# Kernel optimization log

Measured on AMD Instinct MI355X. Metric: run time of the kernel, lower is better.

## Reference

```python
import jax, jax.numpy as jnp
import numpy as np

N_ATOMS = 393216   # 4096 molecules * ~96 atoms
N_FEAT = 128
NB_FILTER = 128
NB_AFFINE = 11     # max_deg(10) + 1 - min_deg(0)
BATCH = 4096


def setup_inputs() -> dict:
    key = jax.random.key(0)
    k1, k2, k3, k4 = jax.random.split(key, 4)
    atoms = jax.random.normal(k1, (N_ATOMS, N_FEAT), jnp.float32)
    # stacked per-degree affine weights (glorot-ish scale)
    W = jax.random.normal(k2, (NB_AFFINE, N_FEAT, NB_FILTER), jnp.float32) / jnp.sqrt(jnp.float32(N_FEAT))
    b = jax.random.normal(k3, (NB_AFFINE, NB_FILTER), jnp.float32) * 0.01
    # contiguous degree layout: deg_slice[k] = (start, count), atoms sorted by degree
    counts = np.full(NB_AFFINE, N_ATOMS // NB_AFFINE, dtype=np.int32)
    counts[-1] += N_ATOMS - counts.sum()
    starts = np.concatenate([[0], np.cumsum(counts)[:-1]]).astype(np.int32)
    deg_slice = jnp.asarray(np.stack([starts, counts], axis=1))  # (11, 2) int32
    membership = jax.random.randint(k4, (N_ATOMS,), 0, BATCH, dtype=jnp.int32)
    return {"atoms": atoms, "W": W, "b": b, "deg_slice": deg_slice,
            "membership": membership, "batch_size": BATCH}


def reference(atoms, W, b, deg_slice, membership, batch_size):
    # atoms: (N, F); W: (K, F, O); b: (K, O); deg_slice: (K, 2)
    n = atoms.shape[0]
    nb_affine = W.shape[0]
    # Per-atom degree index from contiguous deg_slice layout:
    # deg_idx[i] = number of degree blocks that end at or before atom i.
    ends = jnp.cumsum(deg_slice[:, 1])                     # (K,)
    idx = jnp.arange(n, dtype=ends.dtype)
    deg_idx = jnp.sum(idx[:, None] >= ends[None, :], axis=1)  # (N,)
    # Per-degree affine: each atom uses the (W, b) of its degree block.
    out = jnp.zeros((n, W.shape[2]), dtype=atoms.dtype)
    for k in range(nb_affine):  # fixed small structural loop (11 distinct weight sets)
        yk = atoms @ W[k] + b[k]
        out = out + jnp.where((deg_idx == k)[:, None], yk, jnp.zeros((), atoms.dtype))
    # graph_gather: dynamic_partition + per-partition reduce_sum + concat == segment_sum
    pooled = jax.ops.segment_sum(out, membership, num_segments=batch_size)  # (B, O)
    # activation is 'linear' (identity); dropout is None
    return pooled
```

## Files before the change

kernel.cpp:

```cpp
#include <hip/hip_runtime.h>
#include <hip/hip_bf16.h>


#define CAP 64

typedef short bf16x8 __attribute__((ext_vector_type(8)));
typedef float f32x4  __attribute__((ext_vector_type(4)));

__device__ __forceinline__ unsigned short f2bf(float f) {
    unsigned int u = __builtin_bit_cast(unsigned int, f);
    u += 0x7fffu + ((u >> 16) & 1u);
    return (unsigned short)(u >> 16);
}

__device__ __forceinline__ int deg_of(int i, const int* __restrict__ ds, int K) {
    int k = 0, end = 0;
    for (int kk = 0; kk < K; ++kk) { end += ds[2 * kk + 1]; k += (i >= end) ? 1 : 0; }
    return k;
}

__global__ __launch_bounds__(256) void k_fill_wconv(
    const int* __restrict__ mem, const int* __restrict__ ds,
    const float* __restrict__ W,
    unsigned* __restrict__ cnt, unsigned* __restrict__ slots,
    unsigned short* __restrict__ Wb, int N, int K, int nb)
{
    int bx = blockIdx.x;
    if (bx >= nb) {
        __shared__ unsigned short t[128 * 130];
        int k = bx - nb;
        const float* Wk = W + (size_t)k * 16384;
        unsigned short* Wbk = Wb + (size_t)k * 16384;
        for (int e = threadIdx.x; e < 16384; e += 256) {
            int f = e >> 7, c = e & 127;
            t[f * 130 + c] = f2bf(Wk[e]);
        }
        __syncthreads();
        for (int e = threadIdx.x; e < 16384; e += 256) {
            int c = e >> 7, f = e & 127;
            Wbk[e] = t[f * 130 + c];
        }
        return;
    }
    int i = bx * 256 + threadIdx.x;
    if (i >= N) return;
    int key = mem[i] * K + deg_of(i, ds, K);
    unsigned p = atomicAdd(&cnt[key], 1u);
    if (p < CAP) slots[(size_t)key * CAP + p] = (unsigned)i;
}

__device__ __forceinline__ float4 f4add(float4 a, float4 b) {
    return make_float4(a.x + b.x, a.y + b.y, a.z + b.z, a.w + b.w);
}

__global__ __launch_bounds__(256) void k_phaseA(
    const float* __restrict__ atoms,
    const unsigned* __restrict__ cnt,
    const unsigned* __restrict__ slots,
    unsigned short* __restrict__ S, int KB)
{
    int bin = blockIdx.x * 4 + (threadIdx.x >> 6);
    if (bin >= KB) return;
    int lane = threadIdx.x & 63;
    int rpar = lane >> 5;
    int f4   = lane & 31;
    int n = (int)cnt[bin];
    if (n > CAP) n = CAP;
    const unsigned* sl = slots + (size_t)bin * CAP;

    float4 A0 = make_float4(0.f, 0.f, 0.f, 0.f);
    float4 A1 = A0, A2 = A0, A3 = A0;
    int j = rpar;
    for (; j + 6 < n; j += 8) {
        unsigned r0 = sl[j], r1 = sl[j + 2], r2 = sl[j + 4], r3 = sl[j + 6];
        float4 v0 = *reinterpret_cast<const float4*>(atoms + (size_t)r0 * 128 + f4 * 4);
        float4 v1 = *reinterpret_cast<const float4*>(atoms + (size_t)r1 * 128 + f4 * 4);
        float4 v2 = *reinterpret_cast<const float4*>(atoms + (size_t)r2 * 128 + f4 * 4);
        float4 v3 = *reinterpret_cast<const float4*>(atoms + (size_t)r3 * 128 + f4 * 4);
        A0 = f4add(A0, v0); A1 = f4add(A1, v1);
        A2 = f4add(A2, v2); A3 = f4add(A3, v3);
    }
    for (; j < n; j += 2) {
        float4 v = *reinterpret_cast<const float4*>(atoms + (size_t)sl[j] * 128 + f4 * 4);
        A0 = f4add(A0, v);
    }
    float4 Sm = f4add(f4add(A0, A1), f4add(A2, A3));
    Sm.x += __shfl_xor(Sm.x, 32, 64);
    Sm.y += __shfl_xor(Sm.y, 32, 64);
    Sm.z += __shfl_xor(Sm.z, 32, 64);
    Sm.w += __shfl_xor(Sm.w, 32, 64);
    if (rpar == 0) {
        unsigned lo = (unsigned)f2bf(Sm.x) | ((unsigned)f2bf(Sm.y) << 16);
        unsigned hi = (unsigned)f2bf(Sm.z) | ((unsigned)f2bf(Sm.w) << 16);
        *reinterpret_cast<uint2*>(S + (size_t)bin * 128 + f4 * 4) = make_uint2(lo, hi);
    }
}

__global__ __launch_bounds__(64) void k_phaseB(
    const unsigned short* __restrict__ S,
    const unsigned short* __restrict__ Wb,
    const unsigned* __restrict__ cnt,
    const float* __restrict__ bias,
    float* __restrict__ out,
    int K)
{
    int bx   = blockIdx.x;
    int s0   = (bx >> 2) * 16;
    int c0   = (bx & 3) * 32;
    int lane = threadIdx.x;
    int quad = lane >> 4, cb = lane & 15;

    const int KD = K * 128;
    f32x4 acc0 = (f32x4){0.f, 0.f, 0.f, 0.f};
    f32x4 acc1 = (f32x4){0.f, 0.f, 0.f, 0.f};

    const unsigned short* Arow = S  + (size_t)(s0 + cb) * KD + quad * 8;
    const unsigned short* B0   = Wb + (size_t)(c0 + cb)      * 128 + quad * 8;
    const unsigned short* B1   = Wb + (size_t)(c0 + 16 + cb) * 128 + quad * 8;

    #pragma unroll 1
    for (int kk = 0; kk < K; ++kk) {
        #pragma unroll
        for (int k0 = 0; k0 < 128; k0 += 32) {
            bf16x8 a  = *reinterpret_cast<const bf16x8*>(Arow + kk * 128 + k0);
            bf16x8 b0 = *reinterpret_cast<const bf16x8*>(B0 + (size_t)kk * 16384 + k0);
            bf16x8 b1 = *reinterpret_cast<const bf16x8*>(B1 + (size_t)kk * 16384 + k0);
            acc0 = __builtin_amdgcn_mfma_f32_16x16x32_bf16(a, b0, acc0, 0, 0, 0);
            acc1 = __builtin_amdgcn_mfma_f32_16x16x32_bf16(a, b1, acc1, 0, 0, 0);
        }
    }
    #pragma unroll
    for (int reg = 0; reg < 4; ++reg) {
        int s = s0 + quad * 4 + reg;
        float b0s = 0.f, b1s = 0.f;
        for (int k = 0; k < K; ++k) {
            float c = (float)cnt[(size_t)s * K + k];
            b0s += c * bias[k * 128 + c0 + cb];
            b1s += c * bias[k * 128 + c0 + 16 + cb];
        }
        out[(size_t)s * 128 + c0 + cb]      = acc0[reg] + b0s;
        out[(size_t)s * 128 + c0 + 16 + cb] = acc1[reg] + b1s;
    }
}

#define TM 64
#define LDA 136
#define LDW 136
__global__ __launch_bounds__(256, 2) void degree_affine_pool(
    const float* __restrict__ atoms, const float* __restrict__ W,
    const float* __restrict__ bias, const int* __restrict__ deg_slice,
    const int* __restrict__ membership, float* __restrict__ out, int K)
{
    __shared__ unsigned short Alds[TM * LDA];
    __shared__ unsigned short Wlds[128 * LDW];
    const int bid = blockIdx.x, tid = threadIdx.x;
    int k = -1, tile = 0, acc_t = 0;
    for (int kk = 0; kk < K; ++kk) {
        int c = deg_slice[2 * kk + 1];
        int nt = (c + TM - 1) >> 6;
        if (k < 0 && bid < acc_t + nt) { k = kk; tile = bid - acc_t; }
        acc_t += nt;
    }
    if (k < 0) return;
    const int start = deg_slice[2 * k], cnt = deg_slice[2 * k + 1];
    const int row0 = start + tile * TM;
    const int rows_valid = min(TM, cnt - tile * TM);
    for (int e = tid; e < TM * 32; e += 256) {
        int r = e >> 5, f4 = e & 31;
        float4 v = make_float4(0.f, 0.f, 0.f, 0.f);
        if (r < rows_valid)
            v = *reinterpret_cast<const float4*>(atoms + (size_t)(row0 + r) * 128 + f4 * 4);
        unsigned lo = (unsigned)f2bf(v.x) | ((unsigned)f2bf(v.y) << 16);
        unsigned hi = (unsigned)f2bf(v.z) | ((unsigned)f2bf(v.w) << 16);
        *reinterpret_cast<uint2*>(&Alds[r * LDA + f4 * 4]) = make_uint2(lo, hi);
    }
    const float* Wk = W + (size_t)k * 16384;
    for (int e = tid; e < 8192; e += 256) {
        int c = e & 127, f2 = e >> 7;
        unsigned p = (unsigned)f2bf(Wk[(2 * f2) * 128 + c]) |
                     ((unsigned)f2bf(Wk[(2 * f2 + 1) * 128 + c]) << 16);
        *reinterpret_cast<unsigned*>(&Wlds[c * LDW + 2 * f2]) = p;
    }
    __syncthreads();
    const int wave = tid >> 6, lane = tid & 63, quad = lane >> 4, cb = lane & 15;
    f32x4 acc[8];
    #pragma unroll
    for (int ct = 0; ct < 8; ++ct) acc[ct] = (f32x4){0.f, 0.f, 0.f, 0.f};
    #pragma unroll
    for (int k0 = 0; k0 < 128; k0 += 32) {
        bf16x8 af = *reinterpret_cast<const bf16x8*>(&Alds[(wave * 16 + cb) * LDA + k0 + quad * 8]);
        #pragma unroll
        for (int ct = 0; ct < 8; ++ct) {
            bf16x8 bf = *reinterpret_cast<const bf16x8*>(&Wlds[(ct * 16 + cb) * LDW + k0 + quad * 8]);
            acc[ct] = __builtin_amdgcn_mfma_f32_16x16x32_bf16(af, bf, acc[ct], 0, 0, 0);
        }
    }
    int segs[4]; bool valid[4];
    #pragma unroll
    for (int reg = 0; reg < 4; ++reg) {
        int rl = wave * 16 + quad * 4 + reg;
        valid[reg] = (rl < rows_valid);
        segs[reg] = valid[reg] ? membership[row0 + rl] : 0;
    }
    const float* bk = bias + k * 128;
    #pragma unroll
    for (int ct = 0; ct < 8; ++ct) {
        int col = ct * 16 + cb;
        float bv = bk[col];
        #pragma unroll
        for (int reg = 0; reg < 4; ++reg)
            if (valid[reg])
                __hip_atomic_fetch_add(out + (size_t)segs[reg] * 128 + col,
                                       acc[ct][reg] + bv, __ATOMIC_RELAXED,
                                       __HIP_MEMORY_SCOPE_AGENT);
    }
}

static inline size_t aln(size_t x) { return (x + 255) & ~(size_t)255; }

extern "C" void kernel_launch(void* const* d_in, const int* in_sizes, int n_in,
                              void* d_out, int out_size, void* d_ws, size_t ws_size,
                              hipStream_t stream) {
    const float* atoms = (const float*)d_in[0];
    const float* W     = (const float*)d_in[1];
    const float* bias  = (const float*)d_in[2];
    const int*   deg   = (const int*)d_in[3];
    const int*   mem   = (const int*)d_in[4];
    float*       out   = (float*)d_out;

    const int K  = in_sizes[3] / 2;
    const int N  = in_sizes[0] / 128;
    const int B  = out_size / 128;
    const int KB = B * K;

    size_t oWb   = 0;                       size_t sWb   = (size_t)K * 16384 * 2;
    size_t oCnt  = aln(oWb + sWb);          size_t sCnt  = (size_t)KB * 4;
    size_t oSlot = aln(oCnt + sCnt);        size_t sSlot = (size_t)KB * CAP * 4;
    size_t oS    = aln(oSlot + sSlot);      size_t sS    = (size_t)KB * 128 * 2;
    size_t total = oS + sS;

    if (ws_size < total || (B & 15) != 0) {
        (void)hipMemsetAsync(d_out, 0, (size_t)out_size * sizeof(float), stream);
        const int blocks = (N + TM - 1) / TM + K;
        degree_affine_pool<<<blocks, 256, 0, stream>>>(atoms, W, bias, deg, mem, out, K);
        return;
    }

    char* ws = (char*)d_ws;
    unsigned short* Wb    = (unsigned short*)(ws + oWb);
    unsigned*       cnt   = (unsigned*)(ws + oCnt);
    unsigned*       slots = (unsigned*)(ws + oSlot);
    unsigned short* S     = (unsigned short*)(ws + oS);

    (void)hipMemsetAsync(cnt, 0, sCnt, stream);

    const int nb = (N + 255) / 256;
    k_fill_wconv<<<nb + K, 256, 0, stream>>>(mem, deg, W, cnt, slots, Wb, N, K, nb);
    k_phaseA    <<<(KB + 3) / 4, 256, 0, stream>>>(atoms, cnt, slots, S, KB);
    k_phaseB    <<<(B / 16) * 4, 64, 0, stream>>>(S, Wb, cnt, bias, out, K);
}
```

Before: 347.1 us.

## Merge bin, gather, and GEMM phases into one cooperative persistent kernel

Replaces the memset and three separate launches with a single cooperative-launch kernel that uses grid-wide syncs between phases: zeroing counts, binning atoms, converting weights plus gathering bin sums, then an MFMA GEMM with bias folded in from the counts. The aim is to remove launch and inter-kernel gaps. The GEMM phase also writes directly instead of using atomics. The grid is capped at 1024 blocks, so each phase has less parallelism, and the grid syncs add cost. It falls back to the old path if cooperative launch is unavailable.

```diff
diff --git a/kernel.cpp b/kernel.cpp
--- a/kernel.cpp
+++ b/kernel.cpp
@@ -1,5 +1,8 @@
 #include <hip/hip_runtime.h>
 #include <hip/hip_bf16.h>
+#include <hip/hip_cooperative_groups.h>
+
+namespace cg = cooperative_groups;
 
 
 #define CAP 64
@@ -17,6 +20,119 @@
     int k = 0, end = 0;
     for (int kk = 0; kk < K; ++kk) { end += ds[2 * kk + 1]; k += (i >= end) ? 1 : 0; }
     return k;
+}
+
+__device__ __forceinline__ float4 f4add(float4 a, float4 b) {
+    return make_float4(a.x + b.x, a.y + b.y, a.z + b.z, a.w + b.w);
+}
+
+__global__ __launch_bounds__(256, 4) void k_merged(
+    const float* __restrict__ atoms, const float* __restrict__ W,
+    const float* __restrict__ bias, const int* __restrict__ ds,
+    const int* __restrict__ mem,
+    unsigned* __restrict__ cnt, unsigned* __restrict__ slots,
+    unsigned short* __restrict__ Wb, unsigned short* __restrict__ S,
+    float* __restrict__ out, int N, int K, int B, int KB)
+{
+    cg::grid_group gg = cg::this_grid();
+    const int tid  = threadIdx.x;
+    const int gtid = blockIdx.x * 256 + tid;
+    const int gsz  = gridDim.x * 256;
+    const int lane = tid & 63;
+
+    for (int i = gtid; i < KB; i += gsz) cnt[i] = 0u;
+    __threadfence();
+    gg.sync();
+
+    for (int i = gtid; i < N; i += gsz) {
+        int key = mem[i] * K + deg_of(i, ds, K);
+        unsigned p = atomicAdd(&cnt[key], 1u);
+        if (p < CAP) slots[(size_t)key * CAP + p] = (unsigned)i;
+    }
+    __threadfence();
+    gg.sync();
+
+    if (blockIdx.x < (unsigned)K) {
+        __shared__ unsigned short t[128 * 130];
+        const float* Wk = W + (size_t)blockIdx.x * 16384;
+        unsigned short* Wbk = Wb + (size_t)blockIdx.x * 16384;
+        for (int e = tid; e < 16384; e += 256)
+            t[(e >> 7) * 130 + (e & 127)] = f2bf(Wk[e]);
+        __syncthreads();
+        for (int e = tid; e < 16384; e += 256)
+            Wbk[e] = t[(e & 127) * 130 + (e >> 7)];
+    }
+
+    {
+        const int gw   = gtid >> 6;
+        const int nw   = gsz >> 6;
+        const int rpar = lane >> 5;
+        const int f4   = lane & 31;
+        const int bpw  = (KB + nw - 1) / nw;
+        for (int t = 0; t < bpw; ++t) {
+            const int bin = gw * bpw + t;
+            if (bin >= KB) break;
+            int n = (int)cnt[bin];
+            if (n > CAP) n = CAP;
+            const unsigned* sl = slots + (size_t)bin * CAP;
+            float4 A0 = make_float4(0.f, 0.f, 0.f, 0.f);
+            float4 A1 = A0, A2 = A0, A3 = A0;
+            int j = rpar;
+            for (; j + 6 < n; j += 8) {
+                unsigned r0 = sl[j], r1 = sl[j + 2], r2 = sl[j + 4], r3 = sl[j + 6];
+                A0 = f4add(A0, *reinterpret_cast<const float4*>(atoms + (size_t)r0 * 128 + f4 * 4));
+                A1 = f4add(A1, *reinterpret_cast<const float4*>(atoms + (size_t)r1 * 128 + f4 * 4));
+                A2 = f4add(A2, *reinterpret_cast<const float4*>(atoms + (size_t)r2 * 128 + f4 * 4));
+                A3 = f4add(A3, *reinterpret_cast<const float4*>(atoms + (size_t)r3 * 128 + f4 * 4));
+            }
+            for (; j < n; j += 2)
+                A0 = f4add(A0, *reinterpret_cast<const float4*>(atoms + (size_t)sl[j] * 128 + f4 * 4));
+            float4 Sm = f4add(f4add(A0, A1), f4add(A2, A3));
+            Sm.x += __shfl_xor(Sm.x, 32, 64);
+            Sm.y += __shfl_xor(Sm.y, 32, 64);
+            Sm.z += __shfl_xor(Sm.z, 32, 64);
+            Sm.w += __shfl_xor(Sm.w, 32, 64);
+            if (rpar == 0) {
+                unsigned lo = (unsigned)f2bf(Sm.x) | ((unsigned)f2bf(Sm.y) << 16);
+                unsigned hi = (unsigned)f2bf(Sm.z) | ((unsigned)f2bf(Sm.w) << 16);
+                *reinterpret_cast<uint2*>(S + (size_t)bin * 128 + f4 * 4) = make_uint2(lo, hi);
+            }
+        }
+    }
+    __threadfence();
+    gg.sync();
+
+    {
+        const int gw = gtid >> 6;
+        const int nw = gsz >> 6;
+        const int quad = lane >> 4, cb = lane & 15;
+        const int KD = K * 128;
+        const int ntiles = (B >> 4) * 8;
+        for (int tile = gw; tile < ntiles; tile += nw) {
+            const int s0 = (tile >> 3) << 4;
+            const int c0 = (tile & 7) << 4;
+            f32x4 acc = (f32x4){0.f, 0.f, 0.f, 0.f};
+            const unsigned short* Arow = S  + (size_t)(s0 + cb) * KD + quad * 8;
+            const unsigned short* Bp   = Wb + (size_t)(c0 + cb) * 128 + quad * 8;
+            #pragma unroll 1
+            for (int kk = 0; kk < K; ++kk) {
+                #pragma unroll
+                for (int k0 = 0; k0 < 128; k0 += 32) {
+                    bf16x8 a = *reinterpret_cast<const bf16x8*>(Arow + kk * 128 + k0);
+                    bf16x8 b = *reinterpret_cast<const bf16x8*>(Bp + (size_t)kk * 16384 + k0);
+                    acc = __builtin_amdgcn_mfma_f32_16x16x32_bf16(a, b, acc, 0, 0, 0);
+                }
+            }
+            #pragma unroll
+            for (int reg = 0; reg < 4; ++reg) {
+                const int s = s0 + quad * 4 + reg;
+                float bs = 0.f;
+                for (int k = 0; k < K; ++k)
+                    bs += (float)cnt[(size_t)s * K + k] * bias[k * 128 + c0 + cb];
+                out[(size_t)s * 128 + c0 + cb] = acc[reg] + bs;
+            }
+        }
+    }
 }
 
 __global__ __launch_bounds__(256) void k_fill_wconv(
@@ -47,10 +163,6 @@
     int key = mem[i] * K + deg_of(i, ds, K);
     unsigned p = atomicAdd(&cnt[key], 1u);
     if (p < CAP) slots[(size_t)key * CAP + p] = (unsigned)i;
-}
-
-__device__ __forceinline__ float4 f4add(float4 a, float4 b) {
-    return make_float4(a.x + b.x, a.y + b.y, a.z + b.z, a.w + b.w);
 }
 
 __global__ __launch_bounds__(256) void k_phaseA(
@@ -101,8 +213,7 @@
     const unsigned short* __restrict__ Wb,
     const unsigned* __restrict__ cnt,
     const float* __restrict__ bias,
-    float* __restrict__ out,
-    int K)
+    float* __restrict__ out, int K)
 {
     int bx   = blockIdx.x;
     int s0   = (bx >> 2) * 16;
@@ -226,7 +337,7 @@
     const float* bias  = (const float*)d_in[2];
     const int*   deg   = (const int*)d_in[3];
     const int*   mem   = (const int*)d_in[4];
-    float*       out   = (float*)d_out;
+    float*       outp  = (float*)d_out;
 
     const int K  = in_sizes[3] / 2;
     const int N  = in_sizes[0] / 128;
@@ -242,7 +353,7 @@
     if (ws_size < total || (B & 15) != 0) {
         (void)hipMemsetAsync(d_out, 0, (size_t)out_size * sizeof(float), stream);
         const int blocks = (N + TM - 1) / TM + K;
-        degree_affine_pool<<<blocks, 256, 0, stream>>>(atoms, W, bias, deg, mem, out, K);
+        degree_affine_pool<<<blocks, 256, 0, stream>>>(atoms, W, bias, deg, mem, outp, K);
         return;
     }
 
@@ -252,10 +363,36 @@
     unsigned*       slots = (unsigned*)(ws + oSlot);
     unsigned short* S     = (unsigned short*)(ws + oS);
 
+    static int s_grid = -1;
+    if (s_grid < 0) {
+        int dev = 0;  (void)hipGetDevice(&dev);
+        int coop = 0; (void)hipDeviceGetAttribute(&coop, hipDeviceAttributeCooperativeLaunch, dev);
+        int cus = 0;  (void)hipDeviceGetAttribute(&cus, hipDeviceAttributeMultiprocessorCount, dev);
+        int maxb = 0;
+        if (coop) {
+            if (hipOccupancyMaxActiveBlocksPerMultiprocessor(&maxb, k_merged, 256, 0) != hipSuccess)
+                maxb = 0;
+        }
+        int g = (coop && maxb > 0 && cus > 0) ? maxb * cus : 0;
+        if (g > 1024) g = 1024;
+        if (g < 64) g = 0;
+        s_grid = g;
+    }
+
+    if (s_grid > 0) {
+        int Np = N, Kp = K, Bp = B, KBp = KB;
+        void* args[] = { (void*)&atoms, (void*)&W, (void*)&bias, (void*)&deg, (void*)&mem,
+                         (void*)&cnt, (void*)&slots, (void*)&Wb, (void*)&S, (void*)&outp,
+                         (void*)&Np, (void*)&Kp, (void*)&Bp, (void*)&KBp };
+        if (hipLaunchCooperativeKernel(k_merged, dim3(s_grid), dim3(256),
+                                       args, 0u, stream) == hipSuccess)
+            return;
+        s_grid = 0;
+    }
+
     (void)hipMemsetAsync(cnt, 0, sCnt, stream);
-
     const int nb = (N + 255) / 256;
     k_fill_wconv<<<nb + K, 256, 0, stream>>>(mem, deg, W, cnt, slots, Wb, N, K, nb);
     k_phaseA    <<<(KB + 3) / 4, 256, 0, stream>>>(atoms, cnt, slots, S, KB);
-    k_phaseB    <<<(B / 16) * 4, 64, 0, stream>>>(S, Wb, cnt, bias, out, K);
-}
+    k_phaseB    <<<(B / 16) * 4, 64, 0, stream>>>(S, Wb, cnt, bias, outp, K);
+}
```

Result: slower. 820.1 us (+136.3%).

## Split phase-B reduction over degree halves with atomics, zero output in fill kernel

Applied to the files above, without the earlier changes.

Phase B now splits the 11-degree K loop across two blocks per output tile, doubling the grid, and accumulates into the output with relaxed float atomics. The output is zeroed by extra blocks in the fill kernel. Phase A's remainder loop is folded into a predicated main loop, and the W transpose uses half the shared memory in two passes. This trades more parallelism and occupancy for atomic traffic and an extra zeroing pass.

```diff
diff --git a/kernel.cpp b/kernel.cpp
--- a/kernel.cpp
+++ b/kernel.cpp
@@ -19,26 +19,43 @@
     return k;
 }
 
+__device__ __forceinline__ float4 f4add(float4 a, float4 b) {
+    return make_float4(a.x + b.x, a.y + b.y, a.z + b.z, a.w + b.w);
+}
+
 __global__ __launch_bounds__(256) void k_fill_wconv(
     const int* __restrict__ mem, const int* __restrict__ ds,
     const float* __restrict__ W,
     unsigned* __restrict__ cnt, unsigned* __restrict__ slots,
-    unsigned short* __restrict__ Wb, int N, int K, int nb)
+    unsigned short* __restrict__ Wb, float* __restrict__ out,
+    int N, int K, int nb, int B)
 {
     int bx = blockIdx.x;
+    if (bx >= nb + K) {
+        int zb = bx - nb - K;
+        f32x4* o4 = reinterpret_cast<f32x4*>(out);
+        int tot = (B * 128) >> 2;
+        for (int e = zb * 256 + threadIdx.x; e < tot; e += 8 * 256)
+            o4[e] = (f32x4){0.f, 0.f, 0.f, 0.f};
+        return;
+    }
     if (bx >= nb) {
-        __shared__ unsigned short t[128 * 130];
+        __shared__ unsigned short t[64 * 130];
         int k = bx - nb;
         const float* Wk = W + (size_t)k * 16384;
         unsigned short* Wbk = Wb + (size_t)k * 16384;
-        for (int e = threadIdx.x; e < 16384; e += 256) {
-            int f = e >> 7, c = e & 127;
-            t[f * 130 + c] = f2bf(Wk[e]);
-        }
-        __syncthreads();
-        for (int e = threadIdx.x; e < 16384; e += 256) {
-            int c = e >> 7, f = e & 127;
-            Wbk[e] = t[f * 130 + c];
+        #pragma unroll 1
+        for (int h = 0; h < 2; ++h) {
+            for (int e = threadIdx.x; e < 8192; e += 256) {
+                int fl = e >> 7, c = e & 127;
+                t[fl * 130 + c] = f2bf(Wk[(size_t)(h * 64 + fl) * 128 + c]);
+            }
+            __syncthreads();
+            for (int e = threadIdx.x; e < 8192; e += 256) {
+                int c = e >> 6, fl = e & 63;
+                Wbk[(size_t)c * 128 + h * 64 + fl] = t[fl * 130 + c];
+            }
+            __syncthreads();
         }
         return;
     }
@@ -47,10 +64,6 @@
     int key = mem[i] * K + deg_of(i, ds, K);
     unsigned p = atomicAdd(&cnt[key], 1u);
     if (p < CAP) slots[(size_t)key * CAP + p] = (unsigned)i;
-}
-
-__device__ __forceinline__ float4 f4add(float4 a, float4 b) {
-    return make_float4(a.x + b.x, a.y + b.y, a.z + b.z, a.w + b.w);
 }
 
 __global__ __launch_bounds__(256) void k_phaseA(
@@ -68,21 +81,23 @@
     if (n > CAP) n = CAP;
     const unsigned* sl = slots + (size_t)bin * CAP;
 
-    float4 A0 = make_float4(0.f, 0.f, 0.f, 0.f);
-    float4 A1 = A0, A2 = A0, A3 = A0;
-    int j = rpar;
-    for (; j + 6 < n; j += 8) {
-        unsigned r0 = sl[j], r1 = sl[j + 2], r2 = sl[j + 4], r3 = sl[j + 6];
+    const float4 z4 = make_float4(0.f, 0.f, 0.f, 0.f);
+    float4 A0 = z4, A1 = z4, A2 = z4, A3 = z4;
+    for (int j = rpar; j < n; j += 8) {
+        int j1 = j + 2, j2 = j + 4, j3 = j + 6;
+        unsigned r0 = sl[j];
+        unsigned r1 = sl[j1 < n ? j1 : j];
+        unsigned r2 = sl[j2 < n ? j2 : j];
+        unsigned r3 = sl[j3 < n ? j3 : j];
         float4 v0 = *reinterpret_cast<const float4*>(atoms + (size_t)r0 * 128 + f4 * 4);
         float4 v1 = *reinterpret_cast<const float4*>(atoms + (size_t)r1 * 128 + f4 * 4);
         float4 v2 = *reinterpret_cast<const float4*>(atoms + (size_t)r2 * 128 + f4 * 4);
         float4 v3 = *reinterpret_cast<const float4*>(atoms + (size_t)r3 * 128 + f4 * 4);
+        v1 = (j1 < n) ? v1 : z4;
+        v2 = (j2 < n) ? v2 : z4;
+        v3 = (j3 < n) ? v3 : z4;
         A0 = f4add(A0, v0); A1 = f4add(A1, v1);
         A2 = f4add(A2, v2); A3 = f4add(A3, v3);
-    }
-    for (; j < n; j += 2) {
-        float4 v = *reinterpret_cast<const float4*>(atoms + (size_t)sl[j] * 128 + f4 * 4);
-        A0 = f4add(A0, v);
     }
     float4 Sm = f4add(f4add(A0, A1), f4add(A2, A3));
     Sm.x += __shfl_xor(Sm.x, 32, 64);
@@ -96,7 +111,7 @@
     }
 }
 
-__global__ __launch_bounds__(64) void k_phaseB(
+__global__ __launch_bounds__(64) void k_phaseB2(
     const unsigned short* __restrict__ S,
     const unsigned short* __restrict__ Wb,
     const unsigned* __restrict__ cnt,
@@ -105,10 +120,15 @@
     int K)
 {
     int bx   = blockIdx.x;
-    int s0   = (bx >> 2) * 16;
-    int c0   = (bx & 3) * 32;
+    int s0   = (bx >> 3) * 16;
+    int c0   = ((bx >> 1) & 3) * 32;
+    int kh   = bx & 1;
     int lane = threadIdx.x;
     int quad = lane >> 4, cb = lane & 15;
+
+    const int kmid = (K + 1) / 2;
+    const int kbeg = kh ? kmid : 0;
+    const int kend = kh ? K : kmid;
 
     const int KD = K * 128;
     f32x4 acc0 = (f32x4){0.f, 0.f, 0.f, 0.f};
@@ -118,8 +138,8 @@
     const unsigned short* B0   = Wb + (size_t)(c0 + cb)      * 128 + quad * 8;
     const unsigned short* B1   = Wb + (size_t)(c0 + 16 + cb) * 128 + quad * 8;
 
-    #pragma unroll 1
-    for (int kk = 0; kk < K; ++kk) {
+    #pragma unroll 2
+    for (int kk = kbeg; kk < kend; ++kk) {
         #pragma unroll
         for (int k0 = 0; k0 < 128; k0 += 32) {
             bf16x8 a  = *reinterpret_cast<const bf16x8*>(Arow + kk * 128 + k0);
@@ -133,13 +153,17 @@
     for (int reg = 0; reg < 4; ++reg) {
         int s = s0 + quad * 4 + reg;
         float b0s = 0.f, b1s = 0.f;
-        for (int k = 0; k < K; ++k) {
-            float c = (float)cnt[(size_t)s * K + k];
-            b0s += c * bias[k * 128 + c0 + cb];
-            b1s += c * bias[k * 128 + c0 + 16 + cb];
-        }
-        out[(size_t)s * 128 + c0 + cb]      = acc0[reg] + b0s;
-        out[(size_t)s * 128 + c0 + 16 + cb] = acc1[reg] + b1s;
+        if (kh == 0) {
+            for (int k = 0; k < K; ++k) {
+                float c = (float)cnt[(size_t)s * K + k];
+                b0s += c * bias[k * 128 + c0 + cb];
+                b1s += c * bias[k * 128 + c0 + 16 + cb];
+            }
+        }
+        __hip_atomic_fetch_add(out + (size_t)s * 128 + c0 + cb, acc0[reg] + b0s,
+                               __ATOMIC_RELAXED, __HIP_MEMORY_SCOPE_AGENT);
+        __hip_atomic_fetch_add(out + (size_t)s * 128 + c0 + 16 + cb, acc1[reg] + b1s,
+                               __ATOMIC_RELAXED, __HIP_MEMORY_SCOPE_AGENT);
     }
 }
 
@@ -255,7 +279,7 @@
     (void)hipMemsetAsync(cnt, 0, sCnt, stream);
 
     const int nb = (N + 255) / 256;
-    k_fill_wconv<<<nb + K, 256, 0, stream>>>(mem, deg, W, cnt, slots, Wb, N, K, nb);
+    k_fill_wconv<<<nb + K + 8, 256, 0, stream>>>(mem, deg, W, cnt, slots, Wb, out, N, K, nb, B);
     k_phaseA    <<<(KB + 3) / 4, 256, 0, stream>>>(atoms, cnt, slots, S, KB);
-    k_phaseB    <<<(B / 16) * 4, 64, 0, stream>>>(S, Wb, cnt, bias, out, K);
-}
+    k_phaseB2   <<<(B / 16) * 8, 64, 0, stream>>>(S, Wb, cnt, bias, out, K);
+}
```

Measured after the change: 378.3 us. +9.0%, slower.
